# Performance work log

Hardware: AMD Instinct MI355X
Metric: run time of the kernel (lower is better)

## Reference

```python
import jax, jax.numpy as jnp
import numpy as np

B_, H_, N_, L_ = 4, 512, 64, 2048  # batch, d_model, d_state/2 (conj pairs), seq len


def setup_inputs() -> dict:
    key = jax.random.key(0)
    ks = jax.random.split(key, 8)
    x = jax.random.normal(ks[0], (B_, H_, L_), jnp.float32)
    ln_w = jnp.ones((H_,), jnp.float32)
    ln_b = jnp.zeros((H_,), jnp.float32)
    # S4D-style init: dt log-uniform in [1e-3, 1e-1], A = -1/2 + i*pi*n (S4D-Lin)
    log_dt = jax.random.uniform(ks[1], (H_,), jnp.float32) * (np.log(0.1) - np.log(0.001)) + np.log(0.001)
    log_A_real = jnp.broadcast_to(jnp.log(jnp.float32(0.5)), (H_, N_))
    A_imag = jnp.broadcast_to(np.pi * jnp.arange(N_, dtype=np.float32), (H_, N_))
    B_re = jnp.ones((H_, N_), jnp.float32)
    B_im = jnp.zeros((H_, N_), jnp.float32)
    # 2 kernel channels for bidirectional
    C_re = jax.random.normal(ks[2], (2, H_, N_), jnp.float32) * (0.5 ** 0.5)
    C_im = jax.random.normal(ks[3], (2, H_, N_), jnp.float32) * (0.5 ** 0.5)
    D = jax.random.normal(ks[4], (H_,), jnp.float32)
    W_out = jax.random.normal(ks[5], (H_, H_), jnp.float32) / np.sqrt(H_)
    b_out = jnp.zeros((H_,), jnp.float32)
    return dict(x=x, ln_w=ln_w, ln_b=ln_b, log_dt=log_dt, log_A_real=log_A_real,
                A_imag=A_imag, B_re=B_re, B_im=B_im, C_re=C_re, C_im=C_im,
                D=D, W_out=W_out, b_out=b_out)


def _s4_layer(x, ln_w, ln_b, log_dt, log_A_real, A_imag, B_re, B_im, C_re, C_im, D, W_out, b_out):
    Bb, H, L = x.shape
    # ---- pre-norm LayerNorm over channel dim (module transposes to (B,L,H)) ----
    zt = x.transpose(0, 2, 1)                          # (B, L, H)
    mu = zt.mean(-1, keepdims=True)
    var = jnp.mean((zt - mu) ** 2, -1, keepdims=True)
    zt = (zt - mu) * jax.lax.rsqrt(var + 1e-5) * ln_w + ln_b
    z = zt.transpose(0, 2, 1)                          # (B, H, L)
    # ---- S4 diagonal SSM kernel, ZOH discretization, 2 channels (bidirectional) ----
    dt = jnp.exp(log_dt)[:, None]                      # (H, 1)
    A = -jnp.exp(log_A_real) + 1j * A_imag             # (H, N)
    dtA = A * dt                                       # (H, N)
    dB = (B_re + 1j * B_im) * (jnp.exp(dtA) - 1.0) / A # (H, N) discretized B
    CB = (C_re + 1j * C_im) * dB                       # (2, H, N)
    V = jnp.exp(dtA[:, :, None] * jnp.arange(L))       # (H, N, L) Vandermonde exp(l*dt*A)
    k = 2.0 * jnp.real(jnp.einsum('chn,hnl->chl', CB, V))  # (2, H, L)
    # ---- bidirectional: causal + flipped anticausal kernel, length 2L ----
    zpad = jnp.zeros_like(k[0])
    kb = jnp.concatenate([k[0], zpad], -1) + jnp.concatenate([zpad, k[1][:, ::-1]], -1)  # (H, 2L)
    # ---- FFT convolution ----
    k_f = jnp.fft.rfft(kb, n=2 * L)                    # (H, L+1)
    u_f = jnp.fft.rfft(z, n=2 * L)                     # (B, H, L+1)
    y = jnp.fft.irfft(u_f * k_f, n=2 * L)[..., :L]     # (B, H, L)
    y = y + z * D[:, None]                             # skip connection D*u
    y = jax.nn.gelu(y)                                 # default S4 activation
    y = jnp.einsum('oh,bhl->bol', W_out, y) + b_out[:, None]  # output linear (Conv1d k=1)
    return y + x                                       # residual of S4Layer


def reference(x, ln_w, ln_b, log_dt, log_A_real, A_imag, B_re, B_im, C_re, C_im, D, W_out, b_out):
    return _s4_layer(x, ln_w, ln_b, log_dt, log_A_real, A_imag, B_re, B_im, C_re, C_im, D, W_out, b_out)
```

## Files before the change

kernel.cpp:

```cpp
#include <hip/hip_runtime.h>
#include <math.h>

#define Bq 4
#define Hq 512
#define Nq 64
#define Lq 2048
#define PARAM (Hq*Nq)
#define T 64
#define NC (Lq/T)
#define NCOL 256

__global__ void prep_kernel(const float* __restrict__ log_dt,
                            const float* __restrict__ log_A_real,
                            const float* __restrict__ A_imag,
                            const float* __restrict__ B_re, const float* __restrict__ B_im,
                            const float* __restrict__ C_re, const float* __restrict__ C_im,
                            float* __restrict__ a0, float* __restrict__ b0,
                            float* __restrict__ a1, float* __restrict__ b1,
                            float* __restrict__ pw) {
    int idx = blockIdx.x * blockDim.x + threadIdx.x;
    if (idx >= PARAM) return;
    int h = idx >> 6, n = idx & 63;
    float dt = expf(log_dt[h]);
    float Ar = -expf(log_A_real[idx]);
    float Ai = A_imag[idx];
    float er = expf(Ar * dt);
    float wr = er * cosf(Ai * dt);
    float wi = er * sinf(Ai * dt);
    float mr = wr - 1.0f, mi = wi;
    float den = Ar * Ar + Ai * Ai;
    float qr = (mr * Ar + mi * Ai) / den;
    float qi = (mi * Ar - mr * Ai) / den;
    float Br = B_re[idx], Bi = B_im[idx];
    float dBr = Br * qr - Bi * qi;
    float dBi = Br * qi + Bi * qr;
    float cr = C_re[idx], ci = C_im[idx];
    a0[idx] =  2.0f * (cr * dBr - ci * dBi);
    b0[idx] = -2.0f * (cr * dBi + ci * dBr);
    cr = C_re[PARAM + idx]; ci = C_im[PARAM + idx];
    a1[idx] =  2.0f * (cr * dBr - ci * dBi);
    b1[idx] = -2.0f * (cr * dBi + ci * dBr);
    float c = 1.f, s = 0.f;
    float* base = pw + (size_t)h * 65 * 128 + 2 * n;
    for (int d = 0; d <= 64; ++d) {
        *(float2*)(base + (size_t)d * 128) = float2{c, s};
        float nc = c * wr - s * wi;
        float ns = c * wi + s * wr;
        c = nc; s = ns;
    }
}

__global__ __launch_bounds__(128)
void ktap_kernel(const float* __restrict__ pw,
                 const float* __restrict__ a0, const float* __restrict__ b0,
                 const float* __restrict__ a1, const float* __restrict__ b1,
                 float* __restrict__ kt) {
    int h = blockIdx.x;
    int t = threadIdx.x;
    int dir = t >> 6, d = t & 63;
    const float* aa = dir ? a1 : a0;
    const float* bb = dir ? b1 : b0;
    const float* row = pw + (size_t)(h * 65 + d) * 128;
    float acc = 0.f;
    for (int n = 0; n < 64; ++n) {
        float2 v = *(const float2*)(row + 2 * n);
        acc = fmaf(aa[h * 64 + n], v.x, acc);
        acc = fmaf(bb[h * 64 + n], v.y, acc);
    }
    kt[((size_t)h * 2 + dir) * 64 + d] = acc;
}

__global__ __launch_bounds__(256)
void ln_kernel(const float* __restrict__ x, const float* __restrict__ lnw,
               const float* __restrict__ lnb, float* __restrict__ z) {
    int blk = blockIdx.x;
    int b  = blk / (Lq / 16);
    int l0 = (blk % (Lq / 16)) * 16;
    int tx = threadIdx.x & 15;
    int ty = threadIdx.x >> 4;
    const float* xb = x + (size_t)b * Hq * Lq;
    float s = 0.f, s2 = 0.f;
    for (int h = ty; h < Hq; h += 16) {
        float v = xb[h * Lq + l0 + tx];
        s += v; s2 += v * v;
    }
    __shared__ float rs_[16][17], r2_[16][17], mu_s[16], sg_s[16];
    rs_[ty][tx] = s; r2_[ty][tx] = s2;
    __syncthreads();
    if (ty == 0) {
        float a = 0.f, c = 0.f;
        #pragma unroll
        for (int i = 0; i < 16; ++i) { a += rs_[i][tx]; c += r2_[i][tx]; }
        float mu = a * (1.0f / Hq);
        float var = c * (1.0f / Hq) - mu * mu;
        mu_s[tx] = mu;
        sg_s[tx] = rsqrtf(var + 1e-5f);
    }
    __syncthreads();
    float mu = mu_s[tx], rs = sg_s[tx];
    float* zb = z + (size_t)b * Hq * Lq;
    for (int h = ty; h < Hq; h += 16) {
        float v = xb[h * Lq + l0 + tx];
        zb[h * Lq + l0 + tx] = (v - mu) * rs * lnw[h] + lnb[h];
    }
}

__global__ __launch_bounds__(256, 6)
void delta_kernel(const float* __restrict__ z, const float* __restrict__ pw,
                  float* __restrict__ buf) {
    __shared__ float Bs[64][68];
    int h = blockIdx.x, ct = blockIdx.y;
    int t = threadIdx.x;
    int dir = ct >> 1;
    int cc = t & 31, rb = (t >> 5) & 1, jg = t >> 6;
    int b = (ct & 1) * 2 + rb;
    const float* zb = z + ((size_t)b * Hq + h) * Lq;
    if (dir == 0) {
        #pragma unroll
        for (int f = 0; f < 4; ++f) {
            float4 v = *(const float4*)(zb + cc * 64 + 16 * jg + 4 * f);
            Bs[16*jg+4*f+0][rb*32+cc] = v.x;
            Bs[16*jg+4*f+1][rb*32+cc] = v.y;
            Bs[16*jg+4*f+2][rb*32+cc] = v.z;
            Bs[16*jg+4*f+3][rb*32+cc] = v.w;
        }
    } else {
        #pragma unroll
        for (int f = 0; f < 4; ++f) {
            float4 v = *(const float4*)(zb + 2044 - cc * 64 - 16 * jg - 4 * f);
            Bs[16*jg+4*f+3][rb*32+cc] = v.x;
            Bs[16*jg+4*f+2][rb*32+cc] = v.y;
            Bs[16*jg+4*f+1][rb*32+cc] = v.z;
            Bs[16*jg+4*f+0][rb*32+cc] = v.w;
        }
    }
    __syncthreads();
    int tx = t & 15, ty = t >> 4;
    float aR[4][4] = {}, aI[4][4] = {};
    const float* pwh = pw + (size_t)h * 65 * 128;
    #pragma unroll 4
    for (int kk = 0; kk < 64; ++kk) {
        int d = 63 - kk;
        const float4* pr = (const float4*)(pwh + (size_t)d * 128 + 8 * tx);
        float4 p0 = pr[0], p1 = pr[1];
        float4 bv = *(const float4*)&Bs[kk][4 * ty];
        float pc[4] = {p0.x, p0.z, p1.x, p1.z};
        float ps[4] = {p0.y, p0.w, p1.y, p1.w};
        #pragma unroll
        for (int rr = 0; rr < 4; ++rr) {
            #pragma unroll
            for (int q = 0; q < 4; ++q) {
                aR[rr][q] = fmaf(pc[rr], (&bv.x)[q], aR[rr][q]);
                aI[rr][q] = fmaf(ps[rr], (&bv.x)[q], aI[rr][q]);
            }
        }
    }
    #pragma unroll
    for (int q = 0; q < 4; ++q) {
        int colg = ct * 64 + 4 * ty + q;
        float* dst = buf + ((size_t)h * NCOL + colg) * 128 + 8 * tx;
        float4 v1, v2;
        v1.x = aR[0][q]; v1.y = aI[0][q]; v1.z = aR[1][q]; v1.w = aI[1][q];
        v2.x = aR[2][q]; v2.y = aI[2][q]; v2.z = aR[3][q]; v2.w = aI[3][q];
        *(float4*)dst = v1; *(float4*)(dst + 4) = v2;
    }
}

__global__ __launch_bounds__(256)
void cscan_kernel(const float* __restrict__ pw, float* __restrict__ buf) {
    int e = blockIdx.x * 4 + (threadIdx.x >> 6);
    int n = threadIdx.x & 63;
    int h = e >> 3, dir = (e >> 2) & 1, b = e & 3;
    float2 t64 = *(const float2*)(pw + (size_t)(h * 65 + 64) * 128 + 2 * n);
    float tc = t64.x, ts = t64.y;
    float sr = 0.f, si = 0.f;
    float2* p = (float2*)(buf + ((size_t)h * NCOL + dir * 128 + b * 32) * 128) + n;
    float2 d = p[0];
    for (int c = 0; c < NC; ++c) {
        float2 dn;
        if (c + 1 < NC) dn = p[(c + 1) * 64];
        float2 s; s.x = sr; s.y = si;
        p[c * 64] = s;
        float nr = fmaf(tc, sr, fmaf(-ts, si, d.x));
        float ni = fmaf(ts, sr, fmaf(tc, si, d.y));
        sr = nr; si = ni; d = dn;
    }
}

template <int DIR>
__device__ __forceinline__ void y_phases(const float* __restrict__ zb0,
                                         const float* __restrict__ zb1,
                                         const float* __restrict__ pwh,
                                         const float* __restrict__ bufh,
                                         const float* __restrict__ ks,
                                         const float* __restrict__ as_,
                                         const float* __restrict__ bs_,
                                         float (*As)[68], float (*Bs)[68],
                                         int t, int ctB, float acc[4][4]) {
    int tx = t & 15, ty = t >> 4;
    int si = t & 63, sg = t >> 6;
    int cc = t & 31, rb = (t >> 5) & 1, kg = t >> 6;
    const float* zb = rb ? zb1 : zb0;
    const float* prow = pwh + (size_t)(si + ((DIR == 0) ? 1 : 0)) * 128;
    for (int p = 0; p < 6; ++p) {
        if (p < 2) {
            #pragma unroll
            for (int q = 0; q < 8; ++q) {
                int kk = 8 * sg + q;
                int j = 32 * p + kk;
                int idx = (DIR == 0) ? (si - j) : (si - j - 1);
                As[kk][si] = (idx >= 0) ? ks[idx] : 0.f;
            }
        } else {
            #pragma unroll
            for (int q = 0; q < 8; ++q) {
                int kk = 8 * sg + q;
                int m = 32 * (p - 2) + kk;
                int n = m >> 1;
                float2 v = *(const float2*)(prow + 2 * n);
                float av = as_[n], bv = bs_[n];
                As[kk][si] = ((m & 1) == 0) ? fmaf(av, v.x, bv * v.y)
                                            : fmaf(bv, v.x, -av * v.y);
            }
        }
        if (p < 2) {
            if (DIR == 0) {
                #pragma unroll
                for (int f = 0; f < 2; ++f) {
                    float4 v = *(const float4*)(zb + cc * 64 + 32 * p + 8 * kg + 4 * f);
                    Bs[8*kg+4*f+0][rb*32+cc] = v.x;
                    Bs[8*kg+4*f+1][rb*32+cc] = v.y;
                    Bs[8*kg+4*f+2][rb*32+cc] = v.z;
                    Bs[8*kg+4*f+3][rb*32+cc] = v.w;
                }
            } else {
                #pragma unroll
                for (int f = 0; f < 2; ++f) {
                    float4 v = *(const float4*)(zb + 2044 - cc * 64 - 32 * p - 8 * kg - 4 * f);
                    Bs[8*kg+4*f+3][rb*32+cc] = v.x;
                    Bs[8*kg+4*f+2][rb*32+cc] = v.y;
                    Bs[8*kg+4*f+1][rb*32+cc] = v.z;
                    Bs[8*kg+4*f+0][rb*32+cc] = v.w;
                }
            }
        } else {
            int colg = DIR * 128 + ctB * 64 + rb * 32 + cc;
            const float* src = bufh + (size_t)colg * 128 + 32 * (p - 2) + 8 * kg;
            float4 v0 = *(const float4*)src;
            float4 v1 = *(const float4*)(src + 4);
            #pragma unroll
            for (int e2 = 0; e2 < 4; ++e2) Bs[8*kg+e2][rb*32+cc]   = (&v0.x)[e2];
            #pragma unroll
            for (int e2 = 0; e2 < 4; ++e2) Bs[8*kg+4+e2][rb*32+cc] = (&v1.x)[e2];
        }
        __syncthreads();
        #pragma unroll 8
        for (int kk = 0; kk < 32; ++kk) {
            float4 av = *(const float4*)&As[kk][4 * tx];
            float4 bv = *(const float4*)&Bs[kk][4 * ty];
            #pragma unroll
            for (int ii = 0; ii < 4; ++ii) {
                float a = (&av.x)[ii];
                acc[ii][0] = fmaf(a, bv.x, acc[ii][0]);
                acc[ii][1] = fmaf(a, bv.y, acc[ii][1]);
                acc[ii][2] = fmaf(a, bv.z, acc[ii][2]);
                acc[ii][3] = fmaf(a, bv.w, acc[ii][3]);
            }
        }
        __syncthreads();
    }
}

__global__ __launch_bounds__(256, 4)
void yact_kernel(const float* __restrict__ z, const float* __restrict__ pw,
                 const float* __restrict__ a0, const float* __restrict__ b0,
                 const float* __restrict__ a1, const float* __restrict__ b1,
                 const float* __restrict__ kt, const float* __restrict__ buf,
                 const float* __restrict__ Dv, float* __restrict__ u) {
    __shared__ float sh[64 * 68];
    __shared__ float ks0[64], ks1[64], as0[64], bs0[64], as1[64], bs1[64];
    int h = blockIdx.x, ctB = blockIdx.y;
    int t = threadIdx.x;
    if (t < 64) {
        ks0[t] = kt[((size_t)h * 2 + 0) * 64 + t];
        ks1[t] = kt[((size_t)h * 2 + 1) * 64 + t];
        as0[t] = a0[h * 64 + t]; bs0[t] = b0[h * 64 + t];
        as1[t] = a1[h * 64 + t]; bs1[t] = b1[h * 64 + t];
    }
    __syncthreads();
    const float* zb0 = z + ((size_t)(2 * ctB) * Hq + h) * Lq;
    const float* zb1 = z + ((size_t)(2 * ctB + 1) * Hq + h) * Lq;
    const float* pwh = pw + (size_t)h * 65 * 128;
    const float* bufh = buf + (size_t)h * NCOL * 128;
    float (*As)[68] = (float(*)[68])sh;
    float (*Bs)[68] = (float(*)[68])(sh + 32 * 68);
    float acc0[4][4] = {}, acc1[4][4] = {};
    y_phases<0>(zb0, zb1, pwh, bufh, ks0, as0, bs0, As, Bs, t, ctB, acc0);
    y_phases<1>(zb0, zb1, pwh, bufh, ks1, as1, bs1, As, Bs, t, ctB, acc1);
    float (*S1)[68] = (float(*)[68])sh;
    int tx = t & 15, ty = t >> 4;
    #pragma unroll
    for (int q = 0; q < 4; ++q) {
        float4 v;
        v.x = acc1[0][q]; v.y = acc1[1][q]; v.z = acc1[2][q]; v.w = acc1[3][q];
        *(float4*)&S1[4 * ty + q][4 * tx] = v;
    }
    __syncthreads();
    float dv = Dv[h];
    #pragma unroll
    for (int q = 0; q < 4; ++q) {
        int coll = 4 * ty + q;
        int rb2 = coll >> 5, cc2 = coll & 31;
        int b = 2 * ctB + rb2;
        int colrev = rb2 * 32 + (31 - cc2);
        float4 w = *(const float4*)&S1[colrev][60 - 4 * tx];
        size_t base = ((size_t)b * Hq + h) * Lq + cc2 * 64 + 4 * tx;
        float4 zr = *(const float4*)(z + base);
        float vv[4];
        vv[0] = acc0[0][q] + w.w + dv * zr.x;
        vv[1] = acc0[1][q] + w.z + dv * zr.y;
        vv[2] = acc0[2][q] + w.y + dv * zr.z;
        vv[3] = acc0[3][q] + w.x + dv * zr.w;
        #pragma unroll
        for (int i = 0; i < 4; ++i) {
            float v = vv[i];
            float tt = tanhf(0.7978845608028654f * (v + 0.044715f * v * v * v));
            vv[i] = 0.5f * v * (1.0f + tt);
        }
        float4 r; r.x = vv[0]; r.y = vv[1]; r.z = vv[2]; r.w = vv[3];
        *(float4*)(u + base) = r;
    }
}

__global__ __launch_bounds__(512, 4)
void gemm_kernel(const float* __restrict__ u, const float* __restrict__ W,
                 const float* __restrict__ bias, const float* __restrict__ x,
                 float* __restrict__ out) {
    int l0 = blockIdx.x * 64;
    int o0 = blockIdx.y * 128;
    int b  = blockIdx.z;
    int tid = threadIdx.x;
    __shared__ float Ws[2][32][132];
    __shared__ float Us[2][32][68];
    const float* ub = u + (size_t)b * Hq * Lq;
    float acc[4][4] = {};
    int wo = tid >> 4, wl = tid & 15;
    int sj = tid & 31, so = tid >> 5;
    int sl = tid & 63, sk = tid >> 6;
    float wreg[8], ureg[4];
    #pragma unroll
    for (int r = 0; r < 8; ++r) wreg[r] = W[(size_t)(o0 + so + 16*r) * Hq + sj];
    #pragma unroll
    for (int r = 0; r < 4; ++r) ureg[r] = ub[(size_t)(4*sk + r) * Lq + l0 + sl];
    #pragma unroll
    for (int r = 0; r < 8; ++r) Ws[0][sj][so + 16*r] = wreg[r];
    #pragma unroll
    for (int r = 0; r < 4; ++r) Us[0][4*sk + r][sl] = ureg[r];
    __syncthreads();
    for (int t = 0; t < Hq / 32; ++t) {
        int cur = t & 1;
        if (t < 15) {
            int k0 = (t + 1) * 32;
            #pragma unroll
            for (int r = 0; r < 8; ++r)
                wreg[r] = W[(size_t)(o0 + so + 16*r) * Hq + k0 + sj];
            #pragma unroll
            for (int r = 0; r < 4; ++r)
                ureg[r] = ub[(size_t)(k0 + 4*sk + r) * Lq + l0 + sl];
        }
        #pragma unroll 8
        for (int j = 0; j < 32; ++j) {
            float4 av = *(const float4*)&Ws[cur][j][4 * wo];
            float4 bv = *(const float4*)&Us[cur][j][4 * wl];
            #pragma unroll
            for (int io = 0; io < 4; ++io) {
                float a = (&av.x)[io];
                acc[io][0] = fmaf(a, bv.x, acc[io][0]);
                acc[io][1] = fmaf(a, bv.y, acc[io][1]);
                acc[io][2] = fmaf(a, bv.z, acc[io][2]);
                acc[io][3] = fmaf(a, bv.w, acc[io][3]);
            }
        }
        if (t < 15) {
            int nxt = cur ^ 1;
            #pragma unroll
            for (int r = 0; r < 8; ++r) Ws[nxt][sj][so + 16*r] = wreg[r];
            #pragma unroll
            for (int r = 0; r < 4; ++r) Us[nxt][4*sk + r][sl] = ureg[r];
        }
        __syncthreads();
    }
    #pragma unroll
    for (int io = 0; io < 4; ++io) {
        int o = o0 + 4 * wo + io;
        float bo = bias[o];
        size_t base = ((size_t)b * Hq + o) * Lq + l0 + 4 * wl;
        const float4 xr = *(const float4*)(x + base);
        float4 r;
        r.x = acc[io][0] + bo + xr.x;
        r.y = acc[io][1] + bo + xr.y;
        r.z = acc[io][2] + bo + xr.z;
        r.w = acc[io][3] + bo + xr.w;
        *(float4*)(out + base) = r;
    }
}

extern "C" void kernel_launch(void* const* d_in, const int* in_sizes, int n_in,
                              void* d_out, int out_size, void* d_ws, size_t ws_size,
                              hipStream_t stream) {
    (void)in_sizes; (void)n_in; (void)out_size; (void)ws_size;
    const float* x          = (const float*)d_in[0];
    const float* ln_w       = (const float*)d_in[1];
    const float* ln_b       = (const float*)d_in[2];
    const float* log_dt     = (const float*)d_in[3];
    const float* log_A_real = (const float*)d_in[4];
    const float* A_imag     = (const float*)d_in[5];
    const float* B_re       = (const float*)d_in[6];
    const float* B_im       = (const float*)d_in[7];
    const float* C_re       = (const float*)d_in[8];
    const float* C_im       = (const float*)d_in[9];
    const float* Dv         = (const float*)d_in[10];
    const float* W          = (const float*)d_in[11];
    const float* b_out      = (const float*)d_in[12];
    float* out = (float*)d_out;
    float* ws  = (float*)d_ws;

    const size_t BHL = (size_t)Bq * Hq * Lq;
    float* a0  = ws;
    float* b0  = ws + (size_t)PARAM;
    float* a1  = ws + 2 * (size_t)PARAM;
    float* b1  = ws + 3 * (size_t)PARAM;
    float* kt  = ws + 4 * (size_t)PARAM;
    float* pw  = ws + 6 * (size_t)PARAM;
    float* z   = ws + 136 * (size_t)PARAM;
    float* u   = z  + BHL;
    float* buf = u + BHL;

    prep_kernel<<<PARAM / 256, 256, 0, stream>>>(log_dt, log_A_real, A_imag,
                                                 B_re, B_im, C_re, C_im,
                                                 a0, b0, a1, b1, pw);
    ln_kernel<<<Bq * (Lq / 16), 256, 0, stream>>>(x, ln_w, ln_b, z);
    ktap_kernel<<<Hq, 128, 0, stream>>>(pw, a0, b0, a1, b1, kt);
    delta_kernel<<<dim3(Hq, 4), 256, 0, stream>>>(z, pw, buf);
    cscan_kernel<<<Bq * Hq * 2 / 4, 256, 0, stream>>>(pw, buf);
    yact_kernel<<<dim3(Hq, 2), 256, 0, stream>>>(z, pw, a0, b0, a1, b1,
                                                 kt, buf, Dv, u);
    gemm_kernel<<<dim3(Lq / 64, Hq / 128, Bq), 512, 0, stream>>>(u, W, b_out, x, out);
}
```

Baseline: 308.3 us.

## Merge causal and anticausal passes in yact into one K-concatenated GEMM per batch

Restructures yact_kernel so each block handles one (head, batch) pair instead of two batches. The causal and anticausal contributions are folded into one accumulation: the intra-chunk Toeplitz tile combines both kernel taps, and the anticausal state terms are read with reversed chunk and power indexing. This removes the second accumulator set and the shared-memory transpose pass for the reverse direction, halves the per-thread tile to 4x2, and doubles the grid and the occupancy hint. In exchange it runs 10 phases over a narrower 32-column tile, so each block does less register-level reuse of the A tile.

```diff
diff --git a/kernel.cpp b/kernel.cpp
--- a/kernel.cpp
+++ b/kernel.cpp
@@ -187,140 +187,102 @@
     }
 }
 
-template <int DIR>
-__device__ __forceinline__ void y_phases(const float* __restrict__ zb0,
-                                         const float* __restrict__ zb1,
-                                         const float* __restrict__ pwh,
-                                         const float* __restrict__ bufh,
-                                         const float* __restrict__ ks,
-                                         const float* __restrict__ as_,
-                                         const float* __restrict__ bs_,
-                                         float (*As)[68], float (*Bs)[68],
-                                         int t, int ctB, float acc[4][4]) {
-    int tx = t & 15, ty = t >> 4;
-    int si = t & 63, sg = t >> 6;
-    int cc = t & 31, rb = (t >> 5) & 1, kg = t >> 6;
-    const float* zb = rb ? zb1 : zb0;
-    const float* prow = pwh + (size_t)(si + ((DIR == 0) ? 1 : 0)) * 128;
-    for (int p = 0; p < 6; ++p) {
-        if (p < 2) {
-            #pragma unroll
-            for (int q = 0; q < 8; ++q) {
-                int kk = 8 * sg + q;
-                int j = 32 * p + kk;
-                int idx = (DIR == 0) ? (si - j) : (si - j - 1);
-                As[kk][si] = (idx >= 0) ? ks[idx] : 0.f;
-            }
-        } else {
-            #pragma unroll
-            for (int q = 0; q < 8; ++q) {
-                int kk = 8 * sg + q;
-                int m = 32 * (p - 2) + kk;
-                int n = m >> 1;
-                float2 v = *(const float2*)(prow + 2 * n);
-                float av = as_[n], bv = bs_[n];
-                As[kk][si] = ((m & 1) == 0) ? fmaf(av, v.x, bv * v.y)
-                                            : fmaf(bv, v.x, -av * v.y);
-            }
-        }
-        if (p < 2) {
-            if (DIR == 0) {
-                #pragma unroll
-                for (int f = 0; f < 2; ++f) {
-                    float4 v = *(const float4*)(zb + cc * 64 + 32 * p + 8 * kg + 4 * f);
-                    Bs[8*kg+4*f+0][rb*32+cc] = v.x;
-                    Bs[8*kg+4*f+1][rb*32+cc] = v.y;
-                    Bs[8*kg+4*f+2][rb*32+cc] = v.z;
-                    Bs[8*kg+4*f+3][rb*32+cc] = v.w;
-                }
-            } else {
-                #pragma unroll
-                for (int f = 0; f < 2; ++f) {
-                    float4 v = *(const float4*)(zb + 2044 - cc * 64 - 32 * p - 8 * kg - 4 * f);
-                    Bs[8*kg+4*f+3][rb*32+cc] = v.x;
-                    Bs[8*kg+4*f+2][rb*32+cc] = v.y;
-                    Bs[8*kg+4*f+1][rb*32+cc] = v.z;
-                    Bs[8*kg+4*f+0][rb*32+cc] = v.w;
-                }
-            }
-        } else {
-            int colg = DIR * 128 + ctB * 64 + rb * 32 + cc;
-            const float* src = bufh + (size_t)colg * 128 + 32 * (p - 2) + 8 * kg;
-            float4 v0 = *(const float4*)src;
-            float4 v1 = *(const float4*)(src + 4);
-            #pragma unroll
-            for (int e2 = 0; e2 < 4; ++e2) Bs[8*kg+e2][rb*32+cc]   = (&v0.x)[e2];
-            #pragma unroll
-            for (int e2 = 0; e2 < 4; ++e2) Bs[8*kg+4+e2][rb*32+cc] = (&v1.x)[e2];
-        }
-        __syncthreads();
-        #pragma unroll 8
-        for (int kk = 0; kk < 32; ++kk) {
-            float4 av = *(const float4*)&As[kk][4 * tx];
-            float4 bv = *(const float4*)&Bs[kk][4 * ty];
-            #pragma unroll
-            for (int ii = 0; ii < 4; ++ii) {
-                float a = (&av.x)[ii];
-                acc[ii][0] = fmaf(a, bv.x, acc[ii][0]);
-                acc[ii][1] = fmaf(a, bv.y, acc[ii][1]);
-                acc[ii][2] = fmaf(a, bv.z, acc[ii][2]);
-                acc[ii][3] = fmaf(a, bv.w, acc[ii][3]);
-            }
-        }
-        __syncthreads();
-    }
-}
-
-__global__ __launch_bounds__(256, 4)
+__global__ __launch_bounds__(256, 8)
 void yact_kernel(const float* __restrict__ z, const float* __restrict__ pw,
                  const float* __restrict__ a0, const float* __restrict__ b0,
                  const float* __restrict__ a1, const float* __restrict__ b1,
                  const float* __restrict__ kt, const float* __restrict__ buf,
                  const float* __restrict__ Dv, float* __restrict__ u) {
-    __shared__ float sh[64 * 68];
-    __shared__ float ks0[64], ks1[64], as0[64], bs0[64], as1[64], bs1[64];
-    int h = blockIdx.x, ctB = blockIdx.y;
+    __shared__ float As[32][68];
+    __shared__ float Bs[32][36];
+    __shared__ float ks0[64], ks1[64], as0_[64], bs0_[64], as1_[64], bs1_[64];
+    int h = blockIdx.x, b = blockIdx.y;
     int t = threadIdx.x;
     if (t < 64) {
-        ks0[t] = kt[((size_t)h * 2 + 0) * 64 + t];
-        ks1[t] = kt[((size_t)h * 2 + 1) * 64 + t];
-        as0[t] = a0[h * 64 + t]; bs0[t] = b0[h * 64 + t];
-        as1[t] = a1[h * 64 + t]; bs1[t] = b1[h * 64 + t];
-    }
+        ks0[t]  = kt[((size_t)h * 2 + 0) * 64 + t];
+        ks1[t]  = kt[((size_t)h * 2 + 1) * 64 + t];
+        as0_[t] = a0[h * 64 + t]; bs0_[t] = b0[h * 64 + t];
+        as1_[t] = a1[h * 64 + t]; bs1_[t] = b1[h * 64 + t];
+    }
+    int tx = t & 15, ty = t >> 4;
+    int si = t & 63, kkg = t >> 6;
+    int cc = t & 31, kg = t >> 5;
+    const float* zb   = z + ((size_t)b * Hq + h) * Lq;
+    const float* bufh = buf + (size_t)h * NCOL * 128;
+    const float* prow0 = pw + (size_t)(h * 65 + si + 1) * 128;
+    const float* prow1 = pw + (size_t)(h * 65 + 63 - si) * 128;
+    float acc[4][2] = {};
     __syncthreads();
-    const float* zb0 = z + ((size_t)(2 * ctB) * Hq + h) * Lq;
-    const float* zb1 = z + ((size_t)(2 * ctB + 1) * Hq + h) * Lq;
-    const float* pwh = pw + (size_t)h * 65 * 128;
-    const float* bufh = buf + (size_t)h * NCOL * 128;
-    float (*As)[68] = (float(*)[68])sh;
-    float (*Bs)[68] = (float(*)[68])(sh + 32 * 68);
-    float acc0[4][4] = {}, acc1[4][4] = {};
-    y_phases<0>(zb0, zb1, pwh, bufh, ks0, as0, bs0, As, Bs, t, ctB, acc0);
-    y_phases<1>(zb0, zb1, pwh, bufh, ks1, as1, bs1, As, Bs, t, ctB, acc1);
-    float (*S1)[68] = (float(*)[68])sh;
-    int tx = t & 15, ty = t >> 4;
-    #pragma unroll
-    for (int q = 0; q < 4; ++q) {
-        float4 v;
-        v.x = acc1[0][q]; v.y = acc1[1][q]; v.z = acc1[2][q]; v.w = acc1[3][q];
-        *(float4*)&S1[4 * ty + q][4 * tx] = v;
-    }
-    __syncthreads();
+    for (int p = 0; p < 10; ++p) {
+        if (p < 2) {
+            #pragma unroll
+            for (int q = 0; q < 8; ++q) {
+                int kk = 8 * kkg + q;
+                int j = 32 * p + kk;
+                int d = si - j;
+                As[kk][si] = (d >= 0) ? ks0[d] : ks1[-d - 1];
+            }
+        } else if (p < 6) {
+            #pragma unroll
+            for (int q = 0; q < 8; ++q) {
+                int kk = 8 * kkg + q;
+                int m = 32 * (p - 2) + kk;
+                int n = m >> 1;
+                float2 v = *(const float2*)(prow0 + 2 * n);
+                As[kk][si] = ((m & 1) == 0) ? fmaf(as0_[n], v.x, bs0_[n] * v.y)
+                                            : fmaf(bs0_[n], v.x, -as0_[n] * v.y);
+            }
+        } else {
+            #pragma unroll
+            for (int q = 0; q < 8; ++q) {
+                int kk = 8 * kkg + q;
+                int m = 32 * (p - 6) + kk;
+                int n = m >> 1;
+                float2 v = *(const float2*)(prow1 + 2 * n);
+                As[kk][si] = ((m & 1) == 0) ? fmaf(as1_[n], v.x, bs1_[n] * v.y)
+                                            : fmaf(bs1_[n], v.x, -as1_[n] * v.y);
+            }
+        }
+        if (p < 2) {
+            float4 v = *(const float4*)(zb + cc * 64 + 32 * p + 4 * kg);
+            Bs[4*kg+0][cc] = v.x; Bs[4*kg+1][cc] = v.y;
+            Bs[4*kg+2][cc] = v.z; Bs[4*kg+3][cc] = v.w;
+        } else if (p < 6) {
+            int colg = b * 32 + cc;
+            float4 v = *(const float4*)(bufh + (size_t)colg * 128 + 32 * (p - 2) + 4 * kg);
+            Bs[4*kg+0][cc] = v.x; Bs[4*kg+1][cc] = v.y;
+            Bs[4*kg+2][cc] = v.z; Bs[4*kg+3][cc] = v.w;
+        } else {
+            int colg = 128 + b * 32 + (31 - cc);
+            float4 v = *(const float4*)(bufh + (size_t)colg * 128 + 32 * (p - 6) + 4 * kg);
+            Bs[4*kg+0][cc] = v.x; Bs[4*kg+1][cc] = v.y;
+            Bs[4*kg+2][cc] = v.z; Bs[4*kg+3][cc] = v.w;
+        }
+        __syncthreads();
+        #pragma unroll 8
+        for (int kk = 0; kk < 32; ++kk) {
+            float4 av = *(const float4*)&As[kk][4 * tx];
+            float2 bv = *(const float2*)&Bs[kk][2 * ty];
+            #pragma unroll
+            for (int ii = 0; ii < 4; ++ii) {
+                float a = (&av.x)[ii];
+                acc[ii][0] = fmaf(a, bv.x, acc[ii][0]);
+                acc[ii][1] = fmaf(a, bv.y, acc[ii][1]);
+            }
+        }
+        __syncthreads();
+    }
     float dv = Dv[h];
     #pragma unroll
-    for (int q = 0; q < 4; ++q) {
-        int coll = 4 * ty + q;
-        int rb2 = coll >> 5, cc2 = coll & 31;
-        int b = 2 * ctB + rb2;
-        int colrev = rb2 * 32 + (31 - cc2);
-        float4 w = *(const float4*)&S1[colrev][60 - 4 * tx];
+    for (int q = 0; q < 2; ++q) {
+        int cc2 = 2 * ty + q;
         size_t base = ((size_t)b * Hq + h) * Lq + cc2 * 64 + 4 * tx;
         float4 zr = *(const float4*)(z + base);
         float vv[4];
-        vv[0] = acc0[0][q] + w.w + dv * zr.x;
-        vv[1] = acc0[1][q] + w.z + dv * zr.y;
-        vv[2] = acc0[2][q] + w.y + dv * zr.z;
-        vv[3] = acc0[3][q] + w.x + dv * zr.w;
+        vv[0] = acc[0][q] + dv * zr.x;
+        vv[1] = acc[1][q] + dv * zr.y;
+        vv[2] = acc[2][q] + dv * zr.z;
+        vv[3] = acc[3][q] + dv * zr.w;
         #pragma unroll
         for (int i = 0; i < 4; ++i) {
             float v = vv[i];
@@ -443,7 +405,7 @@
     ktap_kernel<<<Hq, 128, 0, stream>>>(pw, a0, b0, a1, b1, kt);
     delta_kernel<<<dim3(Hq, 4), 256, 0, stream>>>(z, pw, buf);
     cscan_kernel<<<Bq * Hq * 2 / 4, 256, 0, stream>>>(pw, buf);
-    yact_kernel<<<dim3(Hq, 2), 256, 0, stream>>>(z, pw, a0, b0, a1, b1,
-                                                 kt, buf, Dv, u);
+    yact_kernel<<<dim3(Hq, Bq), 256, 0, stream>>>(z, pw, a0, b0, a1, b1,
+                                                  kt, buf, Dv, u);
     gemm_kernel<<<dim3(Lq / 64, Hq / 128, Bq), 512, 0, stream>>>(u, W, b_out, x, out);
 }
```

Result: slower. 325.1 us (+5.4%).
